# Kernel tuning notes

Measured on AMD Instinct MI355X. Metric: run time of the kernel, lower is better.

The kernel has to match this reference:

```python
import jax, jax.numpy as jnp
import numpy as np

B, N = 4096, 128
STATE_DIM, GOAL_DIM, OBSTACLE_DIM = 6, 6, 4
VEH = 2 * STATE_DIM + GOAL_DIM  # 18


def setup_inputs() -> dict:
    key = jax.random.key(0)
    ks = jax.random.split(key, 8)
    s = lambda k, shp, fan: jax.random.normal(k, shp, jnp.float32) / np.sqrt(fan)
    return {
        "obs": jax.random.normal(ks[0], (B, 138), jnp.float32),
        "obstacles": jax.random.uniform(ks[1], (B, 5, N), jnp.float32),
        "act": jax.random.normal(ks[2], (B, 2), jnp.float32),
        "ow1": s(ks[3], (22, 256), 22),
        "ob1": jnp.zeros((256,), jnp.float32),
        "ow2": s(ks[4], (256, 256), 256),
        "ob2": jnp.zeros((256,), jnp.float32),
        "qw1": s(ks[5], (396, 256), 396),
        "qb1": jnp.zeros((256,), jnp.float32),
        "qw2": s(ks[6], (256, 256), 256),
        "qb2": jnp.zeros((256,), jnp.float32),
        "qw3": s(ks[7], (256, 1), 256),
        "qb3": jnp.zeros((1,), jnp.float32),
    }


def reference(obs, obstacles, act, ow1, ob1, ow2, ob2, qw1, qb1, qw2, qb2, qw3, qb3):
    # obs: [B, 138]; obstacles: [B, obstacle_dim+1, N]; act: [B, 2]
    veh = obs[:, :VEH]                                 # [B, 18]
    obst_data = obstacles[:, :OBSTACLE_DIM, :]         # [B, 4, N]
    mask = obstacles[:, -1, :]                         # [B, N]
    # per-obstacle features: concat broadcast vehicle state with obstacle data -> [B, N, 22]
    x = jnp.concatenate(
        [jnp.broadcast_to(veh[:, None, :], (veh.shape[0], obst_data.shape[2], VEH)),
         obst_data.transpose(0, 2, 1)], axis=-1)
    # shared obstacle MLP (ReLU on both layers, incl. output_activation)
    h = jax.nn.relu(jnp.einsum("bnf,fh->bnh", x, ow1) + ob1)
    h = jax.nn.relu(jnp.einsum("bnh,hk->bnk", h, ow2) + ob2)  # [B, N, 256]
    # masked sum-pool over obstacle axis
    pooled = jnp.einsum("bnh,bn->bh", h, mask)         # [B, 256]
    comb = jnp.concatenate([obs, pooled, act], axis=-1)  # [B, 396]
    q = jax.nn.relu(comb @ qw1 + qb1)
    q = jax.nn.relu(q @ qw2 + qb2)
    q = q @ qw3 + qb3                                   # [B, 1]
    return jnp.squeeze(q, -1)
```

## Files before the change

kernel.cpp:

```cpp
#include <hip/hip_runtime.h>
#include <hip/hip_bf16.h>


typedef __attribute__((ext_vector_type(8))) short short8;
typedef __attribute__((ext_vector_type(4))) float f32x4;

#define MFMA16(A, B, C) __builtin_amdgcn_mfma_f32_16x16x32_bf16(A, B, C, 0, 0, 0)

__device__ __forceinline__ unsigned short f2b(float f) {
  __hip_bfloat16 h = __float2bfloat16(f);
  return __builtin_bit_cast(unsigned short, h);
}
__device__ __forceinline__ float b2f(unsigned short u) {
  unsigned v = ((unsigned)u) << 16;
  return __builtin_bit_cast(float, v);
}
__device__ __forceinline__ unsigned pk2f(float a, float b) {
  unsigned ua = __builtin_bit_cast(unsigned, a) + 0x8000u;
  unsigned ub = __builtin_bit_cast(unsigned, b) + 0x8000u;
  return __builtin_amdgcn_perm(ub, ua, 0x07060302u);
}

__global__ __launch_bounds__(256) void pack_weights(
    const float* __restrict__ ow1, const float* __restrict__ ow2,
    const float* __restrict__ qw1, const float* __restrict__ qw2,
    unsigned short* __restrict__ ow1q, unsigned short* __restrict__ ow2p,
    unsigned short* __restrict__ qw1h, unsigned short* __restrict__ qw1l,
    unsigned short* __restrict__ qw2h, unsigned short* __restrict__ qw2l) {
  int i = blockIdx.x * 256 + threadIdx.x;
  if (i < 8192) {
    int j = i & 7;
    int l15 = (i >> 3) & 15;
    int quad = (i >> 7) & 3;
    int mt = (i >> 9) & 15;
    int k = quad * 8 + j;
    float v = (k < 22) ? ow1[k * 256 + (mt * 16 + l15)] : 0.f;
    ow1q[i] = f2b(v);
  }
  if (i < 65536) {
    int j = i & 7;
    int n = (i >> 3) & 255;
    int qq = i >> 11;
    int k = (qq >> 2) * 32 + (qq & 3) * 8 + j;
    ow2p[i] = f2b(ow2[k * 256 + n]);
    float w = qw2[k * 256 + n];
    unsigned short h = f2b(w);
    qw2h[i] = h;
    qw2l[i] = f2b(w - b2f(h));
  }
  if (i < 106496) {
    int j = i & 7;
    int n = (i >> 3) & 255;
    int qq = i >> 11;
    int k = (qq >> 2) * 32 + (qq & 3) * 8 + j;
    float w = (k < 396) ? qw1[k * 256 + n] : 0.f;
    unsigned short h = f2b(w);
    qw1h[i] = h;
    qw1l[i] = f2b(w - b2f(h));
  }
}

#define XSTR 40
#define HSTR 264

__global__ __launch_bounds__(512, 4) void obstacle_kernel(
    const float* __restrict__ obs, const float* __restrict__ obstacles,
    const unsigned short* __restrict__ ow1q,
    const unsigned short* __restrict__ ow2p,
    const float* __restrict__ ob1, const float* __restrict__ ob2,
    unsigned short* __restrict__ poolH, unsigned short* __restrict__ poolL) {
  __shared__ unsigned short xs[128 * XSTR];
  __shared__ unsigned short h1[128 * HSTR];
  __shared__ float maskS[128];
  __shared__ unsigned short vehB[32];

  const int b = blockIdx.x;
  const int tid = threadIdx.x;

  if (tid < 18) vehB[tid] = f2b(obs[b * 138 + tid]);
  if (tid < 128) maskS[tid] = obstacles[b * 640 + 512 + tid];
  __syncthreads();

  if (tid < 256) {
    int n = tid >> 1;
    int half = tid & 1;
    unsigned short* wr = &xs[n * XSTR + half * 16];
    if (half == 0) {
      unsigned short r01[16];
#pragma unroll
      for (int k = 0; k < 16; k++) r01[k] = vehB[k];
      *(short8*)(wr + 0) = *(short8*)&r01[0];
      *(short8*)(wr + 8) = *(short8*)&r01[8];
    } else {
      unsigned short r2[8];
      r2[0] = vehB[16];
      r2[1] = vehB[17];
#pragma unroll
      for (int d = 0; d < 4; d++)
        r2[2 + d] = f2b(obstacles[b * 640 + d * 128 + n]);
      r2[6] = 0; r2[7] = 0;
      *(short8*)(wr + 0) = *(short8*)&r2[0];
      short8 z = {0, 0, 0, 0, 0, 0, 0, 0};
      *(short8*)(wr + 8) = z;
    }
  }
  __syncthreads();

  const int wave = tid >> 6;
  const int lane = tid & 63;
  const int quad = lane >> 4;
  const int l15 = lane & 15;

  {
    const unsigned short* wp = &ow1q[wave * 1024 + quad * 128 + l15 * 8];
    short8 wfr[2];
#pragma unroll
    for (int i = 0; i < 2; i++) wfr[i] = *(const short8*)(wp + i * 512);

    const unsigned short* bxp = &xs[l15 * XSTR + quad * 8];
    short8 bx[8];
#pragma unroll
    for (int nt = 0; nt < 8; nt++)
      bx[nt] = *(const short8*)(bxp + nt * 16 * XSTR);

    unsigned short* wrb = &h1[l15 * HSTR + wave * 32 + quad * 4];

#pragma unroll
    for (int i = 0; i < 2; i++) {
      f32x4 cinit = *(const f32x4*)&ob1[wave * 32 + i * 16 + quad * 4];
      f32x4 acc1[8];
#pragma unroll
      for (int nt = 0; nt < 8; nt++) acc1[nt] = MFMA16(wfr[i], bx[nt], cinit);
#pragma unroll
      for (int nt = 0; nt < 8; nt++) {
        float v0 = fmaxf(acc1[nt][0], 0.f);
        float v1 = fmaxf(acc1[nt][1], 0.f);
        float v2 = fmaxf(acc1[nt][2], 0.f);
        float v3 = fmaxf(acc1[nt][3], 0.f);
        uint2 pk;
        pk.x = pk2f(v0, v1);
        pk.y = pk2f(v2, v3);
        *(uint2*)(wrb + nt * 16 * HSTR + i * 16) = pk;
      }
    }
  }
  __syncthreads();

  f32x4 acc[8][2];
#pragma unroll
  for (int t = 0; t < 2; t++) {
    float bv = ob2[wave * 32 + t * 16 + l15];
    f32x4 bvec = {bv, bv, bv, bv};
#pragma unroll
    for (int mt = 0; mt < 8; mt++) acc[mt][t] = bvec;
  }

  const unsigned short* bp = &ow2p[(quad * 256 + wave * 32 + l15) * 8];
  const unsigned short* h1r = &h1[l15 * HSTR + quad * 8];
  short8 bcur[2], bnxt[2];
#pragma unroll
  for (int t = 0; t < 2; t++) bcur[t] = *(const short8*)(bp + t * 128);

#pragma unroll 1
  for (int kb = 0; kb < 8; kb++) {
    if (kb < 7) {
#pragma unroll
      for (int t = 0; t < 2; t++)
        bnxt[t] = *(const short8*)(bp + 8192 + t * 128);
    }
    short8 afr[8];
#pragma unroll
    for (int mt = 0; mt < 8; mt++)
      afr[mt] = *(const short8*)(h1r + mt * 16 * HSTR);
#pragma unroll
    for (int mt = 0; mt < 8; mt++)
#pragma unroll
      for (int t = 0; t < 2; t++) acc[mt][t] = MFMA16(afr[mt], bcur[t], acc[mt][t]);
    bp += 8192;
    h1r += 32;
    if (kb < 7) {
#pragma unroll
      for (int t = 0; t < 2; t++) bcur[t] = bnxt[t];
    }
  }

  f32x4 mk[8];
  const float* mkp = &maskS[quad * 4];
#pragma unroll
  for (int mt = 0; mt < 8; mt++) mk[mt] = *(const f32x4*)(mkp + mt * 16);

#pragma unroll
  for (int t = 0; t < 2; t++) {
    float s = 0.f;
#pragma unroll
    for (int mt = 0; mt < 8; mt++) {
#pragma unroll
      for (int r = 0; r < 4; r++) {
        float v = fmaxf(acc[mt][t][r], 0.f);
        s = fmaf(mk[mt][r], v, s);
      }
    }
    s += __shfl_xor(s, 16);
    s += __shfl_xor(s, 32);
    if (quad == 0) {
      int n = wave * 32 + t * 16 + l15;
      unsigned short sh = (unsigned short)(__builtin_bit_cast(unsigned, s) >> 16);
      poolH[b * 256 + n] = sh;
      poolL[b * 256 + n] = f2b(s - b2f(sh));
    }
  }
}

__global__ __launch_bounds__(1024) void head_mfma(
    const float* __restrict__ obs, const float* __restrict__ act,
    const unsigned short* __restrict__ poolH,
    const unsigned short* __restrict__ poolL,
    const unsigned short* __restrict__ qw1h,
    const unsigned short* __restrict__ qw1l,
    const unsigned short* __restrict__ qw2h,
    const unsigned short* __restrict__ qw2l,
    const float* __restrict__ qb1, const float* __restrict__ qb2,
    const float* __restrict__ qw3, const float* __restrict__ qb3,
    float* __restrict__ out) {
  const int CSTR = 424;
  const int HSTRQ = 264;
  __shared__ unsigned short combH[16 * 424], combL[16 * 424];
  __shared__ unsigned short h1H[16 * 264], h1L[16 * 264];
  __shared__ float wred[16][16];

  const int tid = threadIdx.x;
  const int r0 = blockIdx.x * 16;

  for (int idx = tid; idx < 16 * 416; idx += 1024) {
    int m = idx / 416;
    int k = idx - m * 416;
    unsigned short hi, lo;
    if (k < 138) {
      float v = obs[(r0 + m) * 138 + k];
      hi = f2b(v);
      lo = f2b(v - b2f(hi));
    } else if (k < 394) {
      hi = poolH[(r0 + m) * 256 + (k - 138)];
      lo = poolL[(r0 + m) * 256 + (k - 138)];
    } else if (k < 396) {
      float v = act[(r0 + m) * 2 + (k - 394)];
      hi = f2b(v);
      lo = f2b(v - b2f(hi));
    } else {
      hi = 0; lo = 0;
    }
    combH[m * CSTR + k] = hi;
    combL[m * CSTR + k] = lo;
  }
  __syncthreads();

  const int wave = tid >> 6;
  const int lane = tid & 63;
  const int quad = lane >> 4;
  const int l15 = lane & 15;
  const int n = wave * 16 + l15;

  f32x4 acc = {0.f, 0.f, 0.f, 0.f}, accm = {0.f, 0.f, 0.f, 0.f};
  {
    const unsigned short* b1hp = &qw1h[(quad * 256 + n) * 8];
    const unsigned short* b1lp = &qw1l[(quad * 256 + n) * 8];
    const unsigned short* aHp = &combH[l15 * CSTR + quad * 8];
    const unsigned short* aLp = &combL[l15 * CSTR + quad * 8];
    short8 bh = *(const short8*)b1hp;
    short8 bl = *(const short8*)b1lp;
    short8 bhn, bln;
#pragma unroll 1
    for (int kb = 0; kb < 13; kb++) {
      if (kb < 12) {
        bhn = *(const short8*)(b1hp + 8192);
        bln = *(const short8*)(b1lp + 8192);
      }
      short8 ah = *(const short8*)aHp;
      short8 al = *(const short8*)aLp;
      acc = MFMA16(ah, bh, acc);
      accm = MFMA16(ah, bl, accm);
      accm = MFMA16(al, bh, accm);
      b1hp += 8192; b1lp += 8192; aHp += 32; aLp += 32;
      if (kb < 12) { bh = bhn; bl = bln; }
    }
  }
  {
    float bias = qb1[n];
#pragma unroll
    for (int r = 0; r < 4; r++) {
      int m = quad * 4 + r;
      float v = fmaxf(acc[r] + accm[r] + bias, 0.f);
      unsigned short hi = f2b(v);
      h1H[m * HSTRQ + n] = hi;
      h1L[m * HSTRQ + n] = f2b(v - b2f(hi));
    }
  }
  __syncthreads();

  f32x4 a2 = {0.f, 0.f, 0.f, 0.f}, a2m = {0.f, 0.f, 0.f, 0.f};
  {
    const unsigned short* b2hp = &qw2h[(quad * 256 + n) * 8];
    const unsigned short* b2lp = &qw2l[(quad * 256 + n) * 8];
    const unsigned short* aHp = &h1H[l15 * HSTRQ + quad * 8];
    const unsigned short* aLp = &h1L[l15 * HSTRQ + quad * 8];
    short8 bh = *(const short8*)b2hp;
    short8 bl = *(const short8*)b2lp;
    short8 bhn, bln;
#pragma unroll 1
    for (int kb = 0; kb < 8; kb++) {
      if (kb < 7) {
        bhn = *(const short8*)(b2hp + 8192);
        bln = *(const short8*)(b2lp + 8192);
      }
      short8 ah = *(const short8*)aHp;
      short8 al = *(const short8*)aLp;
      a2 = MFMA16(ah, bh, a2);
      a2m = MFMA16(ah, bl, a2m);
      a2m = MFMA16(al, bh, a2m);
      b2hp += 8192; b2lp += 8192; aHp += 32; aLp += 32;
      if (kb < 7) { bh = bhn; bl = bln; }
    }
  }

  {
    float w3 = qw3[n];
    float qb2n = qb2[n];
#pragma unroll
    for (int r = 0; r < 4; r++) {
      float v = fmaxf(a2[r] + a2m[r] + qb2n, 0.f);
      float s = v * w3;
      s += __shfl_xor(s, 1);
      s += __shfl_xor(s, 2);
      s += __shfl_xor(s, 4);
      s += __shfl_xor(s, 8);
      if (l15 == 0) wred[wave][quad * 4 + r] = s;
    }
  }
  __syncthreads();
  if (tid < 16) {
    float s = qb3[0];
#pragma unroll
    for (int w = 0; w < 16; w++) s += wred[w][tid];
    out[r0 + tid] = s;
  }
}

extern "C" void kernel_launch(void* const* d_in, const int* in_sizes, int n_in,
                              void* d_out, int out_size, void* d_ws, size_t ws_size,
                              hipStream_t stream) {
  const float* obs       = (const float*)d_in[0];
  const float* obstacles = (const float*)d_in[1];
  const float* act       = (const float*)d_in[2];
  const float* ow1       = (const float*)d_in[3];
  const float* ob1       = (const float*)d_in[4];
  const float* ow2       = (const float*)d_in[5];
  const float* ob2       = (const float*)d_in[6];
  const float* qw1       = (const float*)d_in[7];
  const float* qb1       = (const float*)d_in[8];
  const float* qw2       = (const float*)d_in[9];
  const float* qb2       = (const float*)d_in[10];
  const float* qw3       = (const float*)d_in[11];
  const float* qb3       = (const float*)d_in[12];
  float* out = (float*)d_out;

  unsigned short* ow1q = (unsigned short*)d_ws;
  unsigned short* ow2p = ow1q + 8192;
  unsigned short* qw1h = ow2p + 65536;
  unsigned short* qw1l = qw1h + 106496;
  unsigned short* qw2h = qw1l + 106496;
  unsigned short* qw2l = qw2h + 65536;
  unsigned short* poolH = qw2l + 65536;
  unsigned short* poolL = poolH + 1048576;

  pack_weights<<<416, 256, 0, stream>>>(ow1, ow2, qw1, qw2, ow1q, ow2p, qw1h,
                                        qw1l, qw2h, qw2l);
  obstacle_kernel<<<4096, 512, 0, stream>>>(obs, obstacles, ow1q, ow2p, ob1,
                                            ob2, poolH, poolL);
  head_mfma<<<256, 1024, 0, stream>>>(obs, act, poolH, poolL, qw1h, qw1l,
                                      qw2h, qw2l, qb1, qb2, qw3, qb3, out);
}
```

Baseline: 169.7 us.

## Switch obstacle layer-2 GEMM to 32x32x16 MFMA with 2x4 wave tiling

New measurement: 179.2 us. +5.6%, slower.

```diff
diff --git a/kernel.cpp b/kernel.cpp
--- a/kernel.cpp
+++ b/kernel.cpp
@@ -4,8 +4,10 @@
 
 typedef __attribute__((ext_vector_type(8))) short short8;
 typedef __attribute__((ext_vector_type(4))) float f32x4;
+typedef __attribute__((ext_vector_type(16))) float f32x16;
 
 #define MFMA16(A, B, C) __builtin_amdgcn_mfma_f32_16x16x32_bf16(A, B, C, 0, 0, 0)
+#define MFMA32(A, B, C) __builtin_amdgcn_mfma_f32_32x32x16_bf16(A, B, C, 0, 0, 0)
 
 __device__ __forceinline__ unsigned short f2b(float f) {
   __hip_bfloat16 h = __float2bfloat16(f);
@@ -24,7 +26,7 @@
 __global__ __launch_bounds__(256) void pack_weights(
     const float* __restrict__ ow1, const float* __restrict__ ow2,
     const float* __restrict__ qw1, const float* __restrict__ qw2,
-    unsigned short* __restrict__ ow1q, unsigned short* __restrict__ ow2p,
+    unsigned short* __restrict__ ow1q, unsigned short* __restrict__ ow2q,
     unsigned short* __restrict__ qw1h, unsigned short* __restrict__ qw1l,
     unsigned short* __restrict__ qw2h, unsigned short* __restrict__ qw2l) {
   int i = blockIdx.x * 256 + threadIdx.x;
@@ -40,9 +42,12 @@
   if (i < 65536) {
     int j = i & 7;
     int n = (i >> 3) & 255;
+    int hh = (i >> 11) & 1;
+    int ks = i >> 12;
+    int k32 = ks * 16 + hh * 8 + j;
+    ow2q[i] = f2b(ow2[k32 * 256 + n]);
     int qq = i >> 11;
     int k = (qq >> 2) * 32 + (qq & 3) * 8 + j;
-    ow2p[i] = f2b(ow2[k * 256 + n]);
     float w = qw2[k * 256 + n];
     unsigned short h = f2b(w);
     qw2h[i] = h;
@@ -66,11 +71,12 @@
 __global__ __launch_bounds__(512, 4) void obstacle_kernel(
     const float* __restrict__ obs, const float* __restrict__ obstacles,
     const unsigned short* __restrict__ ow1q,
-    const unsigned short* __restrict__ ow2p,
+    const unsigned short* __restrict__ ow2q,
     const float* __restrict__ ob1, const float* __restrict__ ob2,
     unsigned short* __restrict__ poolH, unsigned short* __restrict__ poolL) {
   __shared__ unsigned short xs[128 * XSTR];
   __shared__ unsigned short h1[128 * HSTR];
+  __shared__ float poolP[2][256];
   __shared__ float maskS[128];
   __shared__ unsigned short vehB[32];
 
@@ -146,68 +152,81 @@
   }
   __syncthreads();
 
-  f32x4 acc[8][2];
+  const int wm = wave >> 2;
+  const int wn = wave & 3;
+  const int h32 = lane >> 5;
+  const int l31 = lane & 31;
+
+  f32x16 acc[2][2];
 #pragma unroll
   for (int t = 0; t < 2; t++) {
-    float bv = ob2[wave * 32 + t * 16 + l15];
-    f32x4 bvec = {bv, bv, bv, bv};
-#pragma unroll
-    for (int mt = 0; mt < 8; mt++) acc[mt][t] = bvec;
-  }
-
-  const unsigned short* bp = &ow2p[(quad * 256 + wave * 32 + l15) * 8];
-  const unsigned short* h1r = &h1[l15 * HSTR + quad * 8];
+    float bv = ob2[wn * 64 + t * 32 + l31];
+#pragma unroll
+    for (int mt = 0; mt < 2; mt++)
+#pragma unroll
+      for (int r = 0; r < 16; r++) acc[mt][t][r] = bv;
+  }
+
+  const unsigned short* bp = &ow2q[(h32 * 256 + wn * 64 + l31) * 8];
+  const unsigned short* h1r = &h1[(wm * 64 + l31) * HSTR + h32 * 8];
   short8 bcur[2], bnxt[2];
 #pragma unroll
-  for (int t = 0; t < 2; t++) bcur[t] = *(const short8*)(bp + t * 128);
+  for (int t = 0; t < 2; t++) bcur[t] = *(const short8*)(bp + t * 256);
 
 #pragma unroll 1
-  for (int kb = 0; kb < 8; kb++) {
-    if (kb < 7) {
+  for (int ks = 0; ks < 16; ks++) {
+    if (ks < 15) {
 #pragma unroll
       for (int t = 0; t < 2; t++)
-        bnxt[t] = *(const short8*)(bp + 8192 + t * 128);
-    }
-    short8 afr[8];
-#pragma unroll
-    for (int mt = 0; mt < 8; mt++)
-      afr[mt] = *(const short8*)(h1r + mt * 16 * HSTR);
-#pragma unroll
-    for (int mt = 0; mt < 8; mt++)
-#pragma unroll
-      for (int t = 0; t < 2; t++) acc[mt][t] = MFMA16(afr[mt], bcur[t], acc[mt][t]);
-    bp += 8192;
-    h1r += 32;
-    if (kb < 7) {
+        bnxt[t] = *(const short8*)(bp + 4096 + t * 256);
+    }
+    short8 afr[2];
+#pragma unroll
+    for (int mt = 0; mt < 2; mt++)
+      afr[mt] = *(const short8*)(h1r + mt * 32 * HSTR);
+#pragma unroll
+    for (int mt = 0; mt < 2; mt++)
+#pragma unroll
+      for (int t = 0; t < 2; t++) acc[mt][t] = MFMA32(afr[mt], bcur[t], acc[mt][t]);
+    bp += 4096;
+    h1r += 16;
+    if (ks < 15) {
 #pragma unroll
       for (int t = 0; t < 2; t++) bcur[t] = bnxt[t];
     }
   }
 
-  f32x4 mk[8];
-  const float* mkp = &maskS[quad * 4];
-#pragma unroll
-  for (int mt = 0; mt < 8; mt++) mk[mt] = *(const f32x4*)(mkp + mt * 16);
+  f32x4 mk[2][4];
+#pragma unroll
+  for (int mt = 0; mt < 2; mt++)
+#pragma unroll
+    for (int g = 0; g < 4; g++)
+      mk[mt][g] = *(const f32x4*)&maskS[wm * 64 + mt * 32 + g * 8 + h32 * 4];
 
 #pragma unroll
   for (int t = 0; t < 2; t++) {
     float s = 0.f;
 #pragma unroll
-    for (int mt = 0; mt < 8; mt++) {
-#pragma unroll
-      for (int r = 0; r < 4; r++) {
-        float v = fmaxf(acc[mt][t][r], 0.f);
-        s = fmaf(mk[mt][r], v, s);
+    for (int mt = 0; mt < 2; mt++) {
+#pragma unroll
+      for (int g = 0; g < 4; g++) {
+#pragma unroll
+        for (int j = 0; j < 4; j++) {
+          float v = fmaxf(acc[mt][t][g * 4 + j], 0.f);
+          s = fmaf(mk[mt][g][j], v, s);
+        }
       }
     }
-    s += __shfl_xor(s, 16);
     s += __shfl_xor(s, 32);
-    if (quad == 0) {
-      int n = wave * 32 + t * 16 + l15;
-      unsigned short sh = (unsigned short)(__builtin_bit_cast(unsigned, s) >> 16);
-      poolH[b * 256 + n] = sh;
-      poolL[b * 256 + n] = f2b(s - b2f(sh));
-    }
+    if (h32 == 0) poolP[wm][wn * 64 + t * 32 + l31] = s;
+  }
+  __syncthreads();
+
+  if (tid < 256) {
+    float s = poolP[0][tid] + poolP[1][tid];
+    unsigned short sh = (unsigned short)(__builtin_bit_cast(unsigned, s) >> 16);
+    poolH[b * 256 + tid] = sh;
+    poolL[b * 256 + tid] = f2b(s - b2f(sh));
   }
 }
 
@@ -364,17 +383,17 @@
   float* out = (float*)d_out;
 
   unsigned short* ow1q = (unsigned short*)d_ws;
-  unsigned short* ow2p = ow1q + 8192;
-  unsigned short* qw1h = ow2p + 65536;
+  unsigned short* ow2q = ow1q + 8192;
+  unsigned short* qw1h = ow2q + 65536;
   unsigned short* qw1l = qw1h + 106496;
   unsigned short* qw2h = qw1l + 106496;
   unsigned short* qw2l = qw2h + 65536;
   unsigned short* poolH = qw2l + 65536;
   unsigned short* poolL = poolH + 1048576;
 
-  pack_weights<<<416, 256, 0, stream>>>(ow1, ow2, qw1, qw2, ow1q, ow2p, qw1h,
+  pack_weights<<<416, 256, 0, stream>>>(ow1, ow2, qw1, qw2, ow1q, ow2q, qw1h,
                                         qw1l, qw2h, qw2l);
-  obstacle_kernel<<<4096, 512, 0, stream>>>(obs, obstacles, ow1q, ow2p, ob1,
+  obstacle_kernel<<<4096, 512, 0, stream>>>(obs, obstacles, ow1q, ow2q, ob1,
                                             ob2, poolH, poolL);
   head_mfma<<<256, 1024, 0, stream>>>(obs, act, poolH, poolL, qw1h, qw1l,
                                       qw2h, qw2l, qb1, qb2, qw3, qb3, out);
```
